# Performance work log

Hardware: AMD Instinct MI355X
Metric: run time of the kernel (lower is better)

The kernel has to match this reference:

```python
import jax, jax.numpy as jnp
import numpy as np

EPS = 1e-12
FP8_MAX = 448.0  # torch.finfo(float8_e4m3fn).max
G = 128  # tile/block group size


def per_tile_quant_dequant(x):
    # x: [seq, din]; one scale per 1x128 tile along din (per_tile_quant semantics)
    s, d = x.shape
    xt = x.reshape(s, d // G, G)
    amax = jnp.max(jnp.abs(xt), axis=-1, keepdims=True)
    scale = jnp.maximum(amax, EPS) / FP8_MAX
    q = jnp.clip(xt / scale, -FP8_MAX, FP8_MAX).astype(jnp.float8_e4m3fn)
    return (q.astype(jnp.float32) * scale).reshape(s, d)


def per_block_quant_dequant(w):
    # w: [ne, dout, din]; one scale per 128x128 block
    ne, dout, din = w.shape
    wb = w.reshape(ne, dout // G, G, din // G, G)
    amax = jnp.max(jnp.abs(wb), axis=(2, 4), keepdims=True)
    scale = jnp.maximum(amax, EPS) / FP8_MAX
    q = jnp.clip(wb / scale, -FP8_MAX, FP8_MAX).astype(jnp.float8_e4m3fn)
    return (q.astype(jnp.float32) * scale).reshape(ne, dout, din)


def grouped_gemm(xq, wq, tokens_per_expert):
    # xq: [seq, din] (tokens contiguous per expert); wq: [ne, dout, din]
    seq = xq.shape[0]
    ne, dout, _ = wq.shape
    ends = jnp.cumsum(tokens_per_expert)
    starts = ends - tokens_per_expert
    tok = jnp.arange(seq)
    out = jnp.zeros((seq, dout), dtype=jnp.float32)
    for e in range(ne):  # small fixed expert count
        mask = ((tok >= starts[e]) & (tok < ends[e]))[:, None]
        xe = jnp.where(mask, xq, 0.0)
        out = out + xe @ wq[e].T
    return out


def setup_inputs() -> dict:
    key = jax.random.key(0)
    k1, k2 = jax.random.split(key)
    ne, dout, din, seq = 8, 2048, 2048, 8192
    x = jax.random.normal(k1, (seq, din), dtype=jnp.float32)
    # weight stored flat as (ne*dout, din), as in the module
    weight = jax.random.normal(k2, (ne * dout, din), dtype=jnp.float32) * 0.02
    tokens_per_expert = jnp.full((ne,), seq // ne, dtype=jnp.int32)
    return {"input": x, "weight": weight, "tokens_per_expert": tokens_per_expert}


def reference(input, weight, tokens_per_expert):
    ne, dout, din = 8, 2048, 2048
    w = weight.reshape(ne, dout, din)
    xq = per_tile_quant_dequant(input)          # per-tile fp8 activation quant
    wq = per_block_quant_dequant(w)             # per-block fp8 weight quant
    return grouped_gemm(xq, wq, tokens_per_expert)
```

## Files before the change

kernel.cpp:

```cpp
#include <hip/hip_runtime.h>
#include <hip/hip_bf16.h>
#include <stdint.h>

#define NE   8
#define DOUT 2048
#define DIN  2048
#define SEQ  8192
#define GSZ  128
#define FP8_MAX 448.0f
#define EPSQ 1e-12f

typedef float f32x4  __attribute__((ext_vector_type(4)));
typedef float f32x16 __attribute__((ext_vector_type(16)));
typedef int   i32x4  __attribute__((ext_vector_type(4)));
typedef int   i32x8  __attribute__((ext_vector_type(8)));

__device__ __forceinline__ void async16(void* lds_base, const void* gptr) {
    __builtin_amdgcn_global_load_lds(
        (const __attribute__((address_space(1))) unsigned int*)gptr,
        (__attribute__((address_space(3))) unsigned int*)lds_base,
        16, 0, 0);
}

__global__ __launch_bounds__(256) void quant_x_kernel(
    const float* __restrict__ x, unsigned char* __restrict__ qx,
    float* __restrict__ sx)
{
    const int g = blockIdx.x * 256 + threadIdx.x;
    const float4 v = ((const float4*)x)[g];
    float a = fmaxf(fmaxf(fabsf(v.x), fabsf(v.y)),
                    fmaxf(fabsf(v.z), fabsf(v.w)));
    #pragma unroll
    for (int o = 16; o; o >>= 1) a = fmaxf(a, __shfl_xor(a, o));
    const float scale = fmaxf(a, EPSQ) / FP8_MAX;
    const int tile = g >> 5;
    if ((threadIdx.x & 31) == 0) sx[tile] = scale;

    float q0 = fminf(fmaxf(v.x / scale, -FP8_MAX), FP8_MAX);
    float q1 = fminf(fmaxf(v.y / scale, -FP8_MAX), FP8_MAX);
    float q2 = fminf(fmaxf(v.z / scale, -FP8_MAX), FP8_MAX);
    float q3 = fminf(fmaxf(v.w / scale, -FP8_MAX), FP8_MAX);
    int lo = __builtin_amdgcn_cvt_pk_fp8_f32(q0, q1, 0, false);
    int pk = __builtin_amdgcn_cvt_pk_fp8_f32(q2, q3, lo, true);
    ((unsigned int*)qx)[g] = (unsigned int)pk;
}

__global__ __launch_bounds__(256) void quant_w_kernel(
    const float* __restrict__ w, unsigned char* __restrict__ qw,
    float* __restrict__ sw)
{
    __shared__ float buf[128 * 128];
    __shared__ float red[4];

    const int cb = blockIdx.x;
    const int rb = blockIdx.y;
    const int e  = blockIdx.z;
    const int t  = threadIdx.x;
    const int lane = t & 63, wv = t >> 6;

    const size_t base = ((size_t)e * DOUT + rb * GSZ) * DIN + cb * GSZ;
    const float* wp = w + base;

    #pragma unroll
    for (int j = 0; j < 16; ++j) {
        int f16 = (wv * 16 + j) * 64 + lane;
        int row = f16 >> 5, cc = f16 & 31;
        async16(buf + (wv * 16 + j) * 256,
                wp + (size_t)row * DIN + cc * 4);
    }
    __syncthreads();

    float a = 0.f;
    #pragma unroll
    for (int i = 0; i < 16; ++i) {
        f32x4 v = *(const f32x4*)(buf + (t + i * 256) * 4);
        a = fmaxf(a, fmaxf(fmaxf(fabsf(v[0]), fabsf(v[1])),
                           fmaxf(fabsf(v[2]), fabsf(v[3]))));
    }
    #pragma unroll
    for (int o = 32; o; o >>= 1) a = fmaxf(a, __shfl_xor(a, o));
    if (lane == 0) red[wv] = a;
    __syncthreads();
    a = fmaxf(fmaxf(red[0], red[1]), fmaxf(red[2], red[3]));
    const float scale = fmaxf(a, EPSQ) / FP8_MAX;
    if (t == 0) sw[(e * 16 + rb) * 16 + cb] = scale;

    unsigned int* qout = (unsigned int*)(qw + base);
    #pragma unroll
    for (int i = 0; i < 16; ++i) {
        int idx = t + i * 256;
        f32x4 v = *(const f32x4*)(buf + idx * 4);
        float q0 = fminf(fmaxf(v[0] / scale, -FP8_MAX), FP8_MAX);
        float q1 = fminf(fmaxf(v[1] / scale, -FP8_MAX), FP8_MAX);
        float q2 = fminf(fmaxf(v[2] / scale, -FP8_MAX), FP8_MAX);
        float q3 = fminf(fmaxf(v[3] / scale, -FP8_MAX), FP8_MAX);
        int lo = __builtin_amdgcn_cvt_pk_fp8_f32(q0, q1, 0, false);
        int pk = __builtin_amdgcn_cvt_pk_fp8_f32(q2, q3, lo, true);
        int r = idx >> 5, c4 = idx & 31;
        qout[r * (DIN / 4) + c4] = (unsigned int)pk;
    }
}

__global__ __launch_bounds__(256, 4) void gemm_kernel(
    const unsigned char* __restrict__ qx, const float* __restrict__ sx,
    const unsigned char* __restrict__ qw, const float* __restrict__ sw,
    const int* __restrict__ tpe, float* __restrict__ out)
{
    __shared__ unsigned char Asm[128 * 128];
    __shared__ unsigned char Bsm[128 * 128];
    __shared__ float Rs[16 * 128];

    const int tid  = threadIdx.x;
    const int lane = tid & 63;
    const int wv   = tid >> 6;
    const int wm   = wv >> 1, wn = wv & 1;
    const int l31  = lane & 31;
    const int h    = lane >> 5;
    const int nb   = blockIdx.x;
    const int mb   = blockIdx.y;
    const int r0   = mb * 128, n0 = nb * 128;

    int e = -1, start = 0;
    #pragma unroll
    for (int i = 0; i < NE; ++i) {
        int end = start + tpe[i];
        if (r0 >= start && r0 < end) e = i;
        start = end;
    }
    if (e < 0) {
        f32x4 z = {0.f, 0.f, 0.f, 0.f};
        for (int i = tid; i < 128 * 32; i += 256) {
            int r = i >> 5, c4 = i & 31;
            *(f32x4*)(out + (size_t)(r0 + r) * DOUT + n0 + c4 * 4) = z;
        }
        return;
    }

    {
        float* Cs = (float*)Asm;
        const float* sp  = sx + (size_t)r0 * 16;
        const float* swp = sw + (e * 16 + nb) * 16;
        for (int i = tid; i < 2048; i += 256) {
            int r = i >> 4, kb = i & 15;
            Cs[kb * 128 + r] = sp[i] * swp[kb];
        }
        __syncthreads();
        float rv[8];
        #pragma unroll
        for (int j = 0; j < 8; ++j) {
            int i = tid + j * 256;
            int kb = i >> 7, row = i & 127;
            rv[j] = (kb == 0) ? Cs[15 * 128 + row]
                              : Cs[(kb - 1) * 128 + row] / Cs[kb * 128 + row];
        }
        #pragma unroll
        for (int j = 0; j < 8; ++j) Rs[tid + j * 256] = rv[j];
    }

    const unsigned char* Ag = qx + (size_t)r0 * DIN;
    const unsigned char* Bg = qw + (size_t)e * DOUT * DIN + (size_t)n0 * DIN;

    int srow[4], scol[4];
    #pragma unroll
    for (int j = 0; j < 4; ++j) {
        int f = wv * 4096 + j * 1024 + lane * 16;
        int row = f >> 7, pc = (f >> 4) & 7;
        srow[j] = row;
        scol[j] = (pc ^ (row & 7)) * 16;
    }

    int abase[2], ax8[2], bbase[2], bx8[2];
    #pragma unroll
    for (int i = 0; i < 2; ++i) {
        int ra = wm * 64 + i * 32 + l31;
        abase[i] = ra * 128; ax8[i] = ra & 7;
        int rb = wn * 64 + i * 32 + l31;
        bbase[i] = rb * 128; bx8[i] = rb & 7;
    }

    f32x16 acc[2][2];
    #pragma unroll
    for (int mi = 0; mi < 2; ++mi)
        #pragma unroll
        for (int ni = 0; ni < 2; ++ni)
            #pragma unroll
            for (int q = 0; q < 16; ++q) acc[mi][ni][q] = 0.f;

    for (int kb = 0; kb < 16; ++kb) {
        __syncthreads();
        #pragma unroll
        for (int j = 0; j < 4; ++j) {
            async16(Asm + wv * 4096 + j * 1024,
                    Ag + (size_t)srow[j] * DIN + kb * GSZ + scol[j]);
            async16(Bsm + wv * 4096 + j * 1024,
                    Bg + (size_t)srow[j] * DIN + kb * GSZ + scol[j]);
        }
        __syncthreads();

        if (kb) {
            #pragma unroll
            for (int mi = 0; mi < 2; ++mi) {
                const float* rp = Rs + kb * 128 + wm * 64 + mi * 32 + 4 * h;
                f32x4 rr[4];
                #pragma unroll
                for (int g = 0; g < 4; ++g) rr[g] = *(const f32x4*)(rp + 8 * g);
                #pragma unroll
                for (int ni = 0; ni < 2; ++ni)
                    #pragma unroll
                    for (int g = 0; g < 4; ++g)
                        #pragma unroll
                        for (int j = 0; j < 4; ++j)
                            acc[mi][ni][g * 4 + j] *= rr[g][j];
            }
        }

        #pragma unroll
        for (int ks = 0; ks < 2; ++ks) {
            const int c0 = ks * 4 + h * 2;
            i32x8 A[2], B[2];
            #pragma unroll
            for (int i = 0; i < 2; ++i) {
                i32x4 alo = *(const i32x4*)(Asm + abase[i] + ((c0    ) ^ ax8[i]) * 16);
                i32x4 ahi = *(const i32x4*)(Asm + abase[i] + ((c0 + 1) ^ ax8[i]) * 16);
                i32x4 blo = *(const i32x4*)(Bsm + bbase[i] + ((c0    ) ^ bx8[i]) * 16);
                i32x4 bhi = *(const i32x4*)(Bsm + bbase[i] + ((c0 + 1) ^ bx8[i]) * 16);
                #pragma unroll
                for (int q = 0; q < 4; ++q) {
                    A[i][q] = alo[q]; A[i][q + 4] = ahi[q];
                    B[i][q] = blo[q]; B[i][q + 4] = bhi[q];
                }
            }
            #pragma unroll
            for (int mi = 0; mi < 2; ++mi)
                #pragma unroll
                for (int ni = 0; ni < 2; ++ni)
                    acc[mi][ni] = __builtin_amdgcn_mfma_scale_f32_32x32x64_f8f6f4(
                        A[mi], B[ni], acc[mi][ni],
                        0, 0,
                        0, 0x7f7f7f7f,
                        0, 0x7f7f7f7f);
        }
    }

    #pragma unroll
    for (int mi = 0; mi < 2; ++mi) {
        const float* fp = Rs + wm * 64 + mi * 32 + 4 * h;
        f32x4 fv[4];
        #pragma unroll
        for (int g = 0; g < 4; ++g) fv[g] = *(const f32x4*)(fp + 8 * g);
        const int rbase = r0 + wm * 64 + mi * 32 + 4 * h;
        #pragma unroll
        for (int ni = 0; ni < 2; ++ni) {
            const int col = n0 + wn * 64 + ni * 32 + l31;
            #pragma unroll
            for (int g = 0; g < 4; ++g)
                #pragma unroll
                for (int j = 0; j < 4; ++j)
                    out[(size_t)(rbase + 8 * g + j) * DOUT + col] =
                        acc[mi][ni][g * 4 + j] * fv[g][j];
        }
    }
}

extern "C" void kernel_launch(void* const* d_in, const int* in_sizes, int n_in,
                              void* d_out, int out_size, void* d_ws, size_t ws_size,
                              hipStream_t stream) {
    const float* x   = (const float*)d_in[0];
    const float* wt  = (const float*)d_in[1];
    const int*   tpe = (const int*)d_in[2];
    float* out = (float*)d_out;

    char* ws = (char*)d_ws;
    unsigned char* qx = (unsigned char*)ws;
    unsigned char* qw = qx + (size_t)SEQ * DIN;
    float* sx = (float*)(qw + (size_t)NE * DOUT * DIN);
    float* sw = sx + (size_t)SEQ * 16;

    quant_x_kernel<<<SEQ * DIN / 4 / 256, 256, 0, stream>>>(x, qx, sx);
    quant_w_kernel<<<dim3(16, 16, NE), 256, 0, stream>>>(wt, qw, sw);
    gemm_kernel<<<dim3(DOUT / 128, SEQ / 128), 256, 0, stream>>>(
        qx, sx, qw, sw, tpe, out);
}
```

Before: 297.3 us.

## Use 256x256 GEMM tiles with double-buffered LDS and XCD-aware block mapping

Enlarges the GEMM block tile to 256x256 with 512 threads (8 waves, each owning a 128x64 sub-tile). It double-buffers the A/B LDS tiles so the next k-block's global loads overlap the MFMAs, using explicit vmcnt waits and s_barrier instead of two __syncthreads per step. It remaps block IDs so the blocks on each XCD share M rows, and splits the per-k rescale ratio into activation and weight factors computed from global scales. In exchange it uses much more LDS (over 128KB), which limits occupancy to one block per CU, and launches only 256 blocks.

```diff
diff --git a/kernel.cpp b/kernel.cpp
--- a/kernel.cpp
+++ b/kernel.cpp
@@ -101,24 +101,30 @@
     }
 }
 
-__global__ __launch_bounds__(256, 4) void gemm_kernel(
+__global__ __launch_bounds__(512, 2) void gemm_kernel(
     const unsigned char* __restrict__ qx, const float* __restrict__ sx,
     const unsigned char* __restrict__ qw, const float* __restrict__ sw,
     const int* __restrict__ tpe, float* __restrict__ out)
 {
-    __shared__ unsigned char Asm[128 * 128];
-    __shared__ unsigned char Bsm[128 * 128];
-    __shared__ float Rs[16 * 128];
+    __shared__ __align__(16) unsigned char Asm[2][256 * 128];
+    __shared__ __align__(16) unsigned char Bsm[2][256 * 128];
+    __shared__ __align__(16) float Rs[16 * 256];
+    __shared__ __align__(16) float SwL[2 * 16];
 
     const int tid  = threadIdx.x;
     const int lane = tid & 63;
     const int wv   = tid >> 6;
-    const int wm   = wv >> 1, wn = wv & 1;
+    const int wm   = wv >> 2;
+    const int wn   = wv & 3;
     const int l31  = lane & 31;
     const int h    = lane >> 5;
-    const int nb   = blockIdx.x;
-    const int mb   = blockIdx.y;
-    const int r0   = mb * 128, n0 = nb * 128;
+    const int nh   = wn >> 1;
+
+    const int lid  = blockIdx.x;
+    const int xcd  = lid & 7, t8 = lid >> 3;
+    const int mbid = xcd * 4 + (t8 >> 3);
+    const int nb   = t8 & 7;
+    const int r0   = mbid * 256, n0 = nb * 256;
 
     int e = -1, start = 0;
     #pragma unroll
@@ -129,126 +135,154 @@
     }
     if (e < 0) {
         f32x4 z = {0.f, 0.f, 0.f, 0.f};
-        for (int i = tid; i < 128 * 32; i += 256) {
-            int r = i >> 5, c4 = i & 31;
+        for (int i = tid; i < 256 * 64; i += 512) {
+            int r = i >> 6, c4 = i & 63;
             *(f32x4*)(out + (size_t)(r0 + r) * DOUT + n0 + c4 * 4) = z;
         }
         return;
     }
 
-    {
-        float* Cs = (float*)Asm;
-        const float* sp  = sx + (size_t)r0 * 16;
-        const float* swp = sw + (e * 16 + nb) * 16;
-        for (int i = tid; i < 2048; i += 256) {
-            int r = i >> 4, kb = i & 15;
-            Cs[kb * 128 + r] = sp[i] * swp[kb];
-        }
-        __syncthreads();
-        float rv[8];
-        #pragma unroll
-        for (int j = 0; j < 8; ++j) {
-            int i = tid + j * 256;
-            int kb = i >> 7, row = i & 127;
-            rv[j] = (kb == 0) ? Cs[15 * 128 + row]
-                              : Cs[(kb - 1) * 128 + row] / Cs[kb * 128 + row];
-        }
-        #pragma unroll
-        for (int j = 0; j < 8; ++j) Rs[tid + j * 256] = rv[j];
+    for (int i = tid; i < 16 * 256; i += 512) {
+        int row = i >> 4, kb = i & 15;
+        const float* sp = sx + (size_t)(r0 + row) * 16;
+        Rs[kb * 256 + row] = (kb == 0) ? sp[15] : sp[kb - 1] / sp[kb];
+    }
+    if (tid < 32) {
+        int nhh = tid >> 4, kb = tid & 15;
+        const float* wp = sw + ((e * 16) + (nb * 2 + nhh)) * 16;
+        SwL[nhh * 16 + kb] = (kb == 0) ? wp[15] : wp[kb - 1] / wp[kb];
     }
 
     const unsigned char* Ag = qx + (size_t)r0 * DIN;
     const unsigned char* Bg = qw + (size_t)e * DOUT * DIN + (size_t)n0 * DIN;
 
-    int srow[4], scol[4];
+    int soff[4], ldst[4];
     #pragma unroll
     for (int j = 0; j < 4; ++j) {
         int f = wv * 4096 + j * 1024 + lane * 16;
         int row = f >> 7, pc = (f >> 4) & 7;
-        srow[j] = row;
-        scol[j] = (pc ^ (row & 7)) * 16;
-    }
-
-    int abase[2], ax8[2], bbase[2], bx8[2];
-    #pragma unroll
-    for (int i = 0; i < 2; ++i) {
-        int ra = wm * 64 + i * 32 + l31;
-        abase[i] = ra * 128; ax8[i] = ra & 7;
-        int rb = wn * 64 + i * 32 + l31;
-        bbase[i] = rb * 128; bx8[i] = rb & 7;
-    }
-
-    f32x16 acc[2][2];
-    #pragma unroll
-    for (int mi = 0; mi < 2; ++mi)
+        soff[j] = row * DIN + ((pc ^ (row & 7)) * 16);
+        ldst[j] = wv * 4096 + j * 1024;
+    }
+
+    int abase[4], ax8[4], bbase[2], bx8[2];
+    #pragma unroll
+    for (int mi = 0; mi < 4; ++mi) {
+        int ra = wm * 128 + mi * 32 + l31;
+        abase[mi] = ra * 128; ax8[mi] = ra & 7;
+    }
+    #pragma unroll
+    for (int ni = 0; ni < 2; ++ni) {
+        int rb = wn * 64 + ni * 32 + l31;
+        bbase[ni] = rb * 128; bx8[ni] = rb & 7;
+    }
+
+    #pragma unroll
+    for (int j = 0; j < 4; ++j) {
+        async16(Asm[0] + ldst[j], Ag + soff[j]);
+        async16(Bsm[0] + ldst[j], Bg + soff[j]);
+    }
+    asm volatile("s_waitcnt lgkmcnt(0)" ::: "memory");
+
+    f32x16 acc[4][2];
+    #pragma unroll
+    for (int mi = 0; mi < 4; ++mi)
         #pragma unroll
         for (int ni = 0; ni < 2; ++ni)
             #pragma unroll
             for (int q = 0; q < 16; ++q) acc[mi][ni][q] = 0.f;
 
     for (int kb = 0; kb < 16; ++kb) {
-        __syncthreads();
+        const unsigned char* Ac = Asm[kb & 1];
+        const unsigned char* Bc = Bsm[kb & 1];
+        unsigned char* An = Asm[(kb & 1) ^ 1];
+        unsigned char* Bn = Bsm[(kb & 1) ^ 1];
+        float rwk = 1.f;
+        i32x8 Bf[2][2];
+
         #pragma unroll
-        for (int j = 0; j < 4; ++j) {
-            async16(Asm + wv * 4096 + j * 1024,
-                    Ag + (size_t)srow[j] * DIN + kb * GSZ + scol[j]);
-            async16(Bsm + wv * 4096 + j * 1024,
-                    Bg + (size_t)srow[j] * DIN + kb * GSZ + scol[j]);
-        }
-        __syncthreads();
-
-        if (kb) {
+        for (int p = 0; p < 4; ++p) {
+            if (kb < 15) {
+                async16(An + ldst[p], Ag + soff[p] + (kb + 1) * GSZ);
+                async16(Bn + ldst[p], Bg + soff[p] + (kb + 1) * GSZ);
+            }
+            if (p == 0) {
+                if (kb < 15) asm volatile("s_waitcnt vmcnt(2)" ::: "memory");
+                else         asm volatile("s_waitcnt vmcnt(0)" ::: "memory");
+                __builtin_amdgcn_s_barrier();
+                asm volatile("" ::: "memory");
+            }
+            if (p == 0) {
+                #pragma unroll
+                for (int ks = 0; ks < 2; ++ks) {
+                    const int c0 = ks * 4 + h * 2;
+                    #pragma unroll
+                    for (int ni = 0; ni < 2; ++ni) {
+                        i32x4 lo = *(const i32x4*)(Bc + bbase[ni] + (((c0    ) ^ bx8[ni]) * 16));
+                        i32x4 hi = *(const i32x4*)(Bc + bbase[ni] + (((c0 + 1) ^ bx8[ni]) * 16));
+                        #pragma unroll
+                        for (int q = 0; q < 4; ++q) {
+                            Bf[ks][ni][q] = lo[q]; Bf[ks][ni][q + 4] = hi[q];
+                        }
+                    }
+                }
+                rwk = SwL[nh * 16 + kb];
+            }
+            i32x8 Af[2];
             #pragma unroll
-            for (int mi = 0; mi < 2; ++mi) {
-                const float* rp = Rs + kb * 128 + wm * 64 + mi * 32 + 4 * h;
-                f32x4 rr[4];
-                #pragma unroll
-                for (int g = 0; g < 4; ++g) rr[g] = *(const f32x4*)(rp + 8 * g);
+            for (int ks = 0; ks < 2; ++ks) {
+                const int c0 = ks * 4 + h * 2;
+                i32x4 lo = *(const i32x4*)(Ac + abase[p] + (((c0    ) ^ ax8[p]) * 16));
+                i32x4 hi = *(const i32x4*)(Ac + abase[p] + (((c0 + 1) ^ ax8[p]) * 16));
+                #pragma unroll
+                for (int q = 0; q < 4; ++q) { Af[ks][q] = lo[q]; Af[ks][q + 4] = hi[q]; }
+            }
+            f32x4 rr[4];
+            if (kb) {
+                const float* rp = Rs + kb * 256 + wm * 128 + p * 32 + 4 * h;
+                #pragma unroll
+                for (int g = 0; g < 4; ++g) {
+                    f32x4 t = *(const f32x4*)(rp + 8 * g);
+                    rr[g] = t * rwk;
+                }
+            }
+
+            __builtin_amdgcn_s_barrier();
+            __builtin_amdgcn_s_setprio(1);
+            if (kb) {
                 #pragma unroll
                 for (int ni = 0; ni < 2; ++ni)
                     #pragma unroll
                     for (int g = 0; g < 4; ++g)
                         #pragma unroll
                         for (int j = 0; j < 4; ++j)
-                            acc[mi][ni][g * 4 + j] *= rr[g][j];
-            }
-        }
-
-        #pragma unroll
-        for (int ks = 0; ks < 2; ++ks) {
-            const int c0 = ks * 4 + h * 2;
-            i32x8 A[2], B[2];
+                            acc[p][ni][g * 4 + j] *= rr[g][j];
+            }
             #pragma unroll
-            for (int i = 0; i < 2; ++i) {
-                i32x4 alo = *(const i32x4*)(Asm + abase[i] + ((c0    ) ^ ax8[i]) * 16);
-                i32x4 ahi = *(const i32x4*)(Asm + abase[i] + ((c0 + 1) ^ ax8[i]) * 16);
-                i32x4 blo = *(const i32x4*)(Bsm + bbase[i] + ((c0    ) ^ bx8[i]) * 16);
-                i32x4 bhi = *(const i32x4*)(Bsm + bbase[i] + ((c0 + 1) ^ bx8[i]) * 16);
-                #pragma unroll
-                for (int q = 0; q < 4; ++q) {
-                    A[i][q] = alo[q]; A[i][q + 4] = ahi[q];
-                    B[i][q] = blo[q]; B[i][q + 4] = bhi[q];
-                }
-            }
-            #pragma unroll
-            for (int mi = 0; mi < 2; ++mi)
+            for (int ks = 0; ks < 2; ++ks)
                 #pragma unroll
                 for (int ni = 0; ni < 2; ++ni)
-                    acc[mi][ni] = __builtin_amdgcn_mfma_scale_f32_32x32x64_f8f6f4(
-                        A[mi], B[ni], acc[mi][ni],
+                    acc[p][ni] = __builtin_amdgcn_mfma_scale_f32_32x32x64_f8f6f4(
+                        Af[ks], Bf[ks][ni], acc[p][ni],
                         0, 0,
                         0, 0x7f7f7f7f,
                         0, 0x7f7f7f7f);
+            __builtin_amdgcn_s_setprio(0);
+            __builtin_amdgcn_s_barrier();
         }
     }
 
-    #pragma unroll
-    for (int mi = 0; mi < 2; ++mi) {
-        const float* fp = Rs + wm * 64 + mi * 32 + 4 * h;
+    const float fw = SwL[nh * 16 + 0];
+    #pragma unroll
+    for (int mi = 0; mi < 4; ++mi) {
+        const float* fp = Rs + wm * 128 + mi * 32 + 4 * h;
         f32x4 fv[4];
         #pragma unroll
-        for (int g = 0; g < 4; ++g) fv[g] = *(const f32x4*)(fp + 8 * g);
-        const int rbase = r0 + wm * 64 + mi * 32 + 4 * h;
+        for (int g = 0; g < 4; ++g) {
+            f32x4 t = *(const f32x4*)(fp + 8 * g);
+            fv[g] = t * fw;
+        }
+        const int rbase = r0 + wm * 128 + mi * 32 + 4 * h;
         #pragma unroll
         for (int ni = 0; ni < 2; ++ni) {
             const int col = n0 + wn * 64 + ni * 32 + l31;
@@ -278,6 +312,5 @@
 
     quant_x_kernel<<<SEQ * DIN / 4 / 256, 256, 0, stream>>>(x, qx, sx);
     quant_w_kernel<<<dim3(16, 16, NE), 256, 0, stream>>>(wt, qw, sw);
-    gemm_kernel<<<dim3(DOUT / 128, SEQ / 128), 256, 0, stream>>>(
-        qx, sx, qw, sw, tpe, out);
-}
+    gemm_kernel<<<256, 512, 0, stream>>>(qx, sx, qw, sw, tpe, out);
+}
```

Result: slower. 322.9 us (+8.6%).

## Enlarge GEMM block tile to 256x128 with 512 threads sharing B tile

Applied to the files above, without the earlier changes.

The GEMM block now covers 256 rows instead of 128 using 8 waves (512 threads), so each 128x128 fp8 weight tile loaded into LDS is reused by twice as many activation rows. Load offsets are precomputed, and A fragments are loaded per mi inside the MFMA loop to reduce live registers. The scale-ratio table is resized to 256 rows. This halves weight traffic per output and the number of blocks, in exchange for larger LDS use per block (about 64KB), which may lower occupancy. It also assumes a 256-row block never straddles two experts.

```diff
diff --git a/kernel.cpp b/kernel.cpp
--- a/kernel.cpp
+++ b/kernel.cpp
@@ -101,24 +101,25 @@
     }
 }
 
-__global__ __launch_bounds__(256, 4) void gemm_kernel(
+__global__ __launch_bounds__(512, 4) void gemm_kernel(
     const unsigned char* __restrict__ qx, const float* __restrict__ sx,
     const unsigned char* __restrict__ qw, const float* __restrict__ sw,
     const int* __restrict__ tpe, float* __restrict__ out)
 {
-    __shared__ unsigned char Asm[128 * 128];
-    __shared__ unsigned char Bsm[128 * 128];
-    __shared__ float Rs[16 * 128];
+    __shared__ __align__(16) unsigned char Asm[256 * 128];
+    __shared__ __align__(16) unsigned char Bsm[128 * 128];
+    __shared__ __align__(16) float RsC[16 * 256];
 
     const int tid  = threadIdx.x;
     const int lane = tid & 63;
     const int wv   = tid >> 6;
-    const int wm   = wv >> 1, wn = wv & 1;
+    const int wm   = wv >> 1;
+    const int wn   = wv & 1;
     const int l31  = lane & 31;
     const int h    = lane >> 5;
     const int nb   = blockIdx.x;
     const int mb   = blockIdx.y;
-    const int r0   = mb * 128, n0 = nb * 128;
+    const int r0   = mb * 256, n0 = nb * 128;
 
     int e = -1, start = 0;
     #pragma unroll
@@ -129,7 +130,7 @@
     }
     if (e < 0) {
         f32x4 z = {0.f, 0.f, 0.f, 0.f};
-        for (int i = tid; i < 128 * 32; i += 256) {
+        for (int i = tid; i < 256 * 32; i += 512) {
             int r = i >> 5, c4 = i & 31;
             *(f32x4*)(out + (size_t)(r0 + r) * DOUT + n0 + c4 * 4) = z;
         }
@@ -140,33 +141,40 @@
         float* Cs = (float*)Asm;
         const float* sp  = sx + (size_t)r0 * 16;
         const float* swp = sw + (e * 16 + nb) * 16;
-        for (int i = tid; i < 2048; i += 256) {
-            int r = i >> 4, kb = i & 15;
-            Cs[kb * 128 + r] = sp[i] * swp[kb];
+        for (int i = tid; i < 4096; i += 512) {
+            int row = i >> 4, kb = i & 15;
+            Cs[kb * 256 + row] = sp[i] * swp[kb];
         }
         __syncthreads();
         float rv[8];
         #pragma unroll
         for (int j = 0; j < 8; ++j) {
-            int i = tid + j * 256;
-            int kb = i >> 7, row = i & 127;
-            rv[j] = (kb == 0) ? Cs[15 * 128 + row]
-                              : Cs[(kb - 1) * 128 + row] / Cs[kb * 128 + row];
-        }
-        #pragma unroll
-        for (int j = 0; j < 8; ++j) Rs[tid + j * 256] = rv[j];
+            int i = tid + j * 512;
+            int kb = i >> 8, row = i & 255;
+            rv[j] = (kb == 0) ? Cs[15 * 256 + row]
+                              : Cs[(kb - 1) * 256 + row] / Cs[kb * 256 + row];
+        }
+        #pragma unroll
+        for (int j = 0; j < 8; ++j) RsC[tid + j * 512] = rv[j];
     }
 
     const unsigned char* Ag = qx + (size_t)r0 * DIN;
     const unsigned char* Bg = qw + (size_t)e * DOUT * DIN + (size_t)n0 * DIN;
 
-    int srow[4], scol[4];
+    int sa_off[4], sa_dst[4], sb_off[2], sb_dst[2];
     #pragma unroll
     for (int j = 0; j < 4; ++j) {
         int f = wv * 4096 + j * 1024 + lane * 16;
         int row = f >> 7, pc = (f >> 4) & 7;
-        srow[j] = row;
-        scol[j] = (pc ^ (row & 7)) * 16;
+        sa_off[j] = row * DIN + ((pc ^ (row & 7)) * 16);
+        sa_dst[j] = wv * 4096 + j * 1024;
+    }
+    #pragma unroll
+    for (int j = 0; j < 2; ++j) {
+        int f = wv * 2048 + j * 1024 + lane * 16;
+        int row = f >> 7, pc = (f >> 4) & 7;
+        sb_off[j] = row * DIN + ((pc ^ (row & 7)) * 16);
+        sb_dst[j] = wv * 2048 + j * 1024;
     }
 
     int abase[2], ax8[2], bbase[2], bx8[2];
@@ -189,18 +197,17 @@
     for (int kb = 0; kb < 16; ++kb) {
         __syncthreads();
         #pragma unroll
-        for (int j = 0; j < 4; ++j) {
-            async16(Asm + wv * 4096 + j * 1024,
-                    Ag + (size_t)srow[j] * DIN + kb * GSZ + scol[j]);
-            async16(Bsm + wv * 4096 + j * 1024,
-                    Bg + (size_t)srow[j] * DIN + kb * GSZ + scol[j]);
-        }
+        for (int j = 0; j < 4; ++j)
+            async16(Asm + sa_dst[j], Ag + (size_t)sa_off[j] + kb * GSZ);
+        #pragma unroll
+        for (int j = 0; j < 2; ++j)
+            async16(Bsm + sb_dst[j], Bg + (size_t)sb_off[j] + kb * GSZ);
         __syncthreads();
 
         if (kb) {
             #pragma unroll
             for (int mi = 0; mi < 2; ++mi) {
-                const float* rp = Rs + kb * 128 + wm * 64 + mi * 32 + 4 * h;
+                const float* rp = RsC + kb * 256 + wm * 64 + mi * 32 + 4 * h;
                 f32x4 rr[4];
                 #pragma unroll
                 for (int g = 0; g < 4; ++g) rr[g] = *(const f32x4*)(rp + 8 * g);
@@ -217,34 +224,35 @@
         #pragma unroll
         for (int ks = 0; ks < 2; ++ks) {
             const int c0 = ks * 4 + h * 2;
-            i32x8 A[2], B[2];
-            #pragma unroll
-            for (int i = 0; i < 2; ++i) {
-                i32x4 alo = *(const i32x4*)(Asm + abase[i] + ((c0    ) ^ ax8[i]) * 16);
-                i32x4 ahi = *(const i32x4*)(Asm + abase[i] + ((c0 + 1) ^ ax8[i]) * 16);
-                i32x4 blo = *(const i32x4*)(Bsm + bbase[i] + ((c0    ) ^ bx8[i]) * 16);
-                i32x4 bhi = *(const i32x4*)(Bsm + bbase[i] + ((c0 + 1) ^ bx8[i]) * 16);
-                #pragma unroll
-                for (int q = 0; q < 4; ++q) {
-                    A[i][q] = alo[q]; A[i][q + 4] = ahi[q];
-                    B[i][q] = blo[q]; B[i][q + 4] = bhi[q];
-                }
+            i32x8 Bk[2];
+            #pragma unroll
+            for (int ni = 0; ni < 2; ++ni) {
+                i32x4 lo = *(const i32x4*)(Bsm + bbase[ni] + (((c0    ) ^ bx8[ni]) * 16));
+                i32x4 hi = *(const i32x4*)(Bsm + bbase[ni] + (((c0 + 1) ^ bx8[ni]) * 16));
+                #pragma unroll
+                for (int q = 0; q < 4; ++q) { Bk[ni][q] = lo[q]; Bk[ni][q + 4] = hi[q]; }
             }
             #pragma unroll
-            for (int mi = 0; mi < 2; ++mi)
+            for (int mi = 0; mi < 2; ++mi) {
+                i32x8 Af;
+                i32x4 alo = *(const i32x4*)(Asm + abase[mi] + (((c0    ) ^ ax8[mi]) * 16));
+                i32x4 ahi = *(const i32x4*)(Asm + abase[mi] + (((c0 + 1) ^ ax8[mi]) * 16));
+                #pragma unroll
+                for (int q = 0; q < 4; ++q) { Af[q] = alo[q]; Af[q + 4] = ahi[q]; }
                 #pragma unroll
                 for (int ni = 0; ni < 2; ++ni)
                     acc[mi][ni] = __builtin_amdgcn_mfma_scale_f32_32x32x64_f8f6f4(
-                        A[mi], B[ni], acc[mi][ni],
+                        Af, Bk[ni], acc[mi][ni],
                         0, 0,
                         0, 0x7f7f7f7f,
                         0, 0x7f7f7f7f);
+            }
         }
     }
 
     #pragma unroll
     for (int mi = 0; mi < 2; ++mi) {
-        const float* fp = Rs + wm * 64 + mi * 32 + 4 * h;
+        const float* fp = RsC + wm * 64 + mi * 32 + 4 * h;
         f32x4 fv[4];
         #pragma unroll
         for (int g = 0; g < 4; ++g) fv[g] = *(const f32x4*)(fp + 8 * g);
@@ -278,6 +286,6 @@
 
     quant_x_kernel<<<SEQ * DIN / 4 / 256, 256, 0, stream>>>(x, qx, sx);
     quant_w_kernel<<<dim3(16, 16, NE), 256, 0, stream>>>(wt, qw, sw);
-    gemm_kernel<<<dim3(DOUT / 128, SEQ / 128), 256, 0, stream>>>(
+    gemm_kernel<<<dim3(DOUT / 128, SEQ / 256), 512, 0, stream>>>(
         qx, sx, qw, sw, tpe, out);
 }
```

Measured after the change: 297.4 us. About the same (+0.0%).
